# Optimization experiments

Measured on AMD Instinct MI355X. Metric: run time of the kernel, lower is better.

## Reference

```python
import jax, jax.numpy as jnp
import numpy as np

B, C, H, W = 32, 256, 32, 32


def setup_inputs() -> dict:
    key = jax.random.key(0)
    k1, k2, k3 = jax.random.split(key, 3)
    h = jax.random.normal(k1, (B, C, H, W), dtype=jnp.float32)
    w1_w = jax.random.normal(k2, (1, C), dtype=jnp.float32) * (1.0 / np.sqrt(C))
    w1_b = jnp.zeros((1,), dtype=jnp.float32)
    w2_w = jax.random.normal(k3, (1, C), dtype=jnp.float32) * (1.0 / np.sqrt(C))
    w2_b = jnp.zeros((1,), dtype=jnp.float32)
    return {"h": h, "w1_w": w1_w, "w1_b": w1_b, "w2_w": w2_w, "w2_b": w2_b}


def reference(h, w1_w, w1_b, w2_w, w2_b):
    b, c, hh, ww = h.shape
    x = jnp.transpose(h, (0, 2, 3, 1))            # [B,H,W,C]
    # scalar projections of every spatial token
    a = jnp.einsum('bhwc,c->bhw', x, w1_w[0]) + w1_b[0]   # query-side scalar [B,H,W]
    k = jnp.einsum('bhwc,c->bhw', x, w2_w[0]) + w2_b[0]   # key-side scalar   [B,H,W]
    n = hh * ww
    # additive attention scores over all spatial pairs: [B,H,W,HW]
    scores = jnp.tanh(a[:, :, :, None] + k.reshape(b, 1, 1, n))
    attn = jax.nn.softmax(scores, axis=-1)                 # exp(tanh)/sum == softmax(tanh)
    ctx = jnp.einsum('bijn,bnc->bijc', attn, x.reshape(b, n, c))  # [B,H,W,C]
    out = jnp.where(ctx >= 0, ctx, 0.2 * ctx)              # LeakyReLU(0.2)
    return jnp.transpose(out, (0, 3, 1, 2))                # [B,C,H,W]
```

## Files before the change

### kernel.cpp

```cpp
#include <hip/hip_runtime.h>

constexpr int Bn = 32;
constexpr int Cn = 256;
constexpr int Nn = 1024;

constexpr float C2 = 2.8853900817779268f;
constexpr float K1 = 1.4426950408889634f;

typedef __bf16 v8bf  __attribute__((ext_vector_type(8)));
typedef float  v16f  __attribute__((ext_vector_type(16)));


__global__ __launch_bounds__(512) void prep_kernel(
    const float* __restrict__ h,
    const float* __restrict__ w1, const float* __restrict__ w1b,
    const float* __restrict__ w2, const float* __restrict__ w2b,
    float* __restrict__ pa_g, float* __restrict__ q_g,
    unsigned char* __restrict__ hbf)
{
    int blk = blockIdx.x;
    int xcd = blk & 7, idx = blk >> 3;
    int b   = xcd * 4 + (idx >> 4);
    int n0  = (idx & 15) * 64;
    int t = threadIdx.x, w = t >> 6, l = t & 63;
    int co = l >> 3, oct = l & 7;

    __shared__ float p1[8][64], p2[8][64];

    float s1[8], s2[8];
#pragma unroll
    for (int j = 0; j < 8; ++j) { s1[j] = 0.f; s2[j] = 0.f; }

    const float* hb = h + (size_t)b * Cn * Nn + n0 + oct * 8;
    int nt32 = (n0 >> 5) + (oct >> 2);
    unsigned char* nt_base = hbf + (size_t)(b * 32 + nt32) * 16384;
    int g = oct & 3;

#pragma unroll
    for (int it = 0; it < 4; ++it) {
        int c = it * 64 + w * 8 + co;
        const float* src = hb + (size_t)c * Nn;
        float4 va = *(const float4*)src;
        float4 vb = *(const float4*)(src + 4);
        float w1c = w1[c], w2c = w2[c];
        float v[8] = {va.x, va.y, va.z, va.w, vb.x, vb.y, vb.z, vb.w};
        union { __bf16 bx[8]; uint4 u4; } pk;
#pragma unroll
        for (int j = 0; j < 8; ++j) {
            s1[j] = fmaf(v[j], w1c, s1[j]);
            s2[j] = fmaf(v[j], w2c, s2[j]);
            pk.bx[j] = (__bf16)v[j];
        }
        *(uint4*)(nt_base + c * 64 + ((g ^ (c & 3)) << 4)) = pk.u4;
    }

#pragma unroll
    for (int m = 8; m <= 32; m <<= 1) {
#pragma unroll
        for (int j = 0; j < 8; ++j) {
            s1[j] += __shfl_xor(s1[j], m);
            s2[j] += __shfl_xor(s2[j], m);
        }
    }
    if (co == 0) {
#pragma unroll
        for (int j = 0; j < 8; ++j) {
            p1[w][oct * 8 + j] = s1[j];
            p2[w][oct * 8 + j] = s2[j];
        }
    }
    __syncthreads();
    if (t < 64) {
        float a = w1b[0], k = w2b[0];
#pragma unroll
        for (int ww = 0; ww < 8; ++ww) { a += p1[ww][t]; k += p2[ww][t]; }
        pa_g[b * Nn + n0 + t] = exp2f(C2 * a);
        q_g [b * Nn + n0 + t] = exp2f(C2 * k);
    }
}

constexpr int EST_OFF  = 0;
constexpr int QS_OFF   = 16384;
constexpr int SP_OFF   = 65792;
constexpr int SINV_OFF = 67840;
constexpr int CTX_SMEM = 68096;

__global__ __launch_bounds__(512, 4) void ctx_kernel(
    const unsigned char* __restrict__ hbf,
    const float* __restrict__ pa_g, const float* __restrict__ q_g,
    float* __restrict__ out)
{
    __shared__ alignas(16) unsigned char smem[CTX_SMEM];
    float* qs           = (float*)(smem + QS_OFF);
    float (*Sp)[64]     = (float(*)[64])(smem + SP_OFF);
    float* Sinv         = (float*)(smem + SINV_OFF);
    float (*comb)[257]  = (float(*)[257])smem;

    int blk = blockIdx.x;
    int xcd = blk & 7, slot = blk >> 3;
    int b   = xcd * 4 + (slot >> 4);
    int i0  = (slot & 15) * 64;

    int t = threadIdx.x, w = t >> 6, l = t & 63;
    int lm = l & 31, lh = l >> 5;
    int cq = w & 3, wq = w >> 2;

    const unsigned char* hbf_b = hbf + (size_t)b * 524288;

    for (int i = t; i < Nn; i += 512) qs[i] = q_g[b * Nn + i];
    float pav = pa_g[b * Nn + i0 + l];

    v16f acc[2][2];
#pragma unroll
    for (int x = 0; x < 2; ++x)
#pragma unroll
        for (int y = 0; y < 2; ++y)
#pragma unroll
            for (int r = 0; r < 16; ++r) acc[x][y][r] = 0.f;
    float Spart = 0.f;

    int est_sw = l * 128 + ((w ^ (l & 7)) << 4);

    int cB   = cq * 64 + lm;
    int m4   = cB & 3;
    int off0 = cB * 64 + ((lh ^ m4) << 4);
    int off1 = cB * 64 + (((2 + lh) ^ m4) << 4);

    __syncthreads();
    for (int tt = 0; tt < 16; ++tt) {
        unsigned char* est_base = smem + EST_OFF + ((tt & 1) << 13);
        const unsigned char* pt = hbf_b + (size_t)((wq << 4) + tt) * 16384;
        v8bf b00 = *(const v8bf*)(pt + off0);
        v8bf b01 = *(const v8bf*)(pt + off0 + 2048);
        v8bf b10 = *(const v8bf*)(pt + off1);
        v8bf b11 = *(const v8bf*)(pt + off1 + 2048);
        {
            int qb = wq * 512 + tt * 32 + cq * 8;
            float4 q0 = *(const float4*)&qs[qb];
            float4 q1 = *(const float4*)&qs[qb + 4];
            float qv[8] = {q0.x, q0.y, q0.z, q0.w, q1.x, q1.y, q1.z, q1.w};
            v8bf ev;
#pragma unroll
            for (int j = 0; j < 8; ++j) {
                float z = pav * qv[j];
                float r = __builtin_amdgcn_rcpf(1.f + z);
                float e = exp2f(fmaf(r, -2.f * K1, K1));
                __bf16 eb = (__bf16)e;
                ev[j] = eb;
                Spart += (float)eb;
            }
            *(v8bf*)(est_base + est_sw) = ev;
        }
        __syncthreads();
#pragma unroll
        for (int ks = 0; ks < 2; ++ks) {
            int gA = ((wq << 2) + (ks << 1) + lh) ^ (lm & 7);
            v8bf a0 = *(const v8bf*)(est_base + lm * 128        + (gA << 4));
            v8bf a1 = *(const v8bf*)(est_base + (32 + lm) * 128 + (gA << 4));
            v8bf b0 = ks ? b10 : b00;
            v8bf b1 = ks ? b11 : b01;
            acc[0][0] = __builtin_amdgcn_mfma_f32_32x32x16_bf16(a0, b0, acc[0][0], 0, 0, 0);
            acc[0][1] = __builtin_amdgcn_mfma_f32_32x32x16_bf16(a0, b1, acc[0][1], 0, 0, 0);
            acc[1][0] = __builtin_amdgcn_mfma_f32_32x32x16_bf16(a1, b0, acc[1][0], 0, 0, 0);
            acc[1][1] = __builtin_amdgcn_mfma_f32_32x32x16_bf16(a1, b1, acc[1][1], 0, 0, 0);
        }
    }

    Sp[w][l] = Spart;
    __syncthreads();
    if (t < 64) {
        float S = 0.f;
#pragma unroll
        for (int ww = 0; ww < 8; ++ww) S += Sp[ww][t];
        Sinv[t] = 1.f / S;
    }
    if (wq == 1) {
#pragma unroll
        for (int x = 0; x < 2; ++x)
#pragma unroll
            for (int y = 0; y < 2; ++y)
#pragma unroll
                for (int r = 0; r < 16; ++r) {
                    int rl = (r & 3) + 8 * (r >> 2) + 4 * lh;
                    comb[x * 32 + rl][cq * 64 + y * 32 + lm] = acc[x][y][r];
                }
    }
    __syncthreads();
    if (wq == 0) {
#pragma unroll
        for (int x = 0; x < 2; ++x)
#pragma unroll
            for (int y = 0; y < 2; ++y)
#pragma unroll
                for (int r = 0; r < 16; ++r) {
                    int rl  = (r & 3) + 8 * (r >> 2) + 4 * lh;
                    int row = x * 32 + rl;
                    int col = cq * 64 + y * 32 + lm;
                    float v = (acc[x][y][r] + comb[row][col]) * Sinv[row];
                    v = (v >= 0.f) ? v : 0.2f * v;
                    comb[row][col] = v;
                }
    }
    __syncthreads();
    float* ob = out + (size_t)b * Cn * Nn + i0;
#pragma unroll
    for (int p = 0; p < 8; ++p) {
        int slot = t + (p << 9);
        int c    = slot >> 4;
        int i4   = (slot & 15) << 2;
        float4 o;
        o.x = comb[i4 + 0][c];
        o.y = comb[i4 + 1][c];
        o.z = comb[i4 + 2][c];
        o.w = comb[i4 + 3][c];
        *(float4*)(ob + (size_t)c * Nn + i4) = o;
    }
}

extern "C" void kernel_launch(void* const* d_in, const int* in_sizes, int n_in,
                              void* d_out, int out_size, void* d_ws, size_t ws_size,
                              hipStream_t stream) {
    const float* h   = (const float*)d_in[0];
    const float* w1w = (const float*)d_in[1];
    const float* w1b = (const float*)d_in[2];
    const float* w2w = (const float*)d_in[3];
    const float* w2b = (const float*)d_in[4];
    float* out = (float*)d_out;

    float* pa_ws = (float*)d_ws;
    float* q_ws  = pa_ws + Bn * Nn;
    unsigned char* hbf = (unsigned char*)d_ws + 262144;

    prep_kernel<<<512, 512, 0, stream>>>(h, w1w, w1b, w2w, w2b, pa_ws, q_ws, hbf);
    ctx_kernel <<<512, 512, 0, stream>>>(hbf, pa_ws, q_ws, out);
}
```

Before: 120.1 us.

## Fuse prep and ctx kernels with per-batch atomic flag barrier

Merges the projection/bf16-conversion kernel and the attention-context kernel into one launch. Each batch has an atomic counter that its 16 blocks increment after writing their prep outputs, and each block spins (with sleep and a guard limit) until all 16 arrive. This removes one kernel launch and the gap between kernels. In exchange it adds a memset launch, spin-wait latency, and a dependence on all 16 blocks of a batch being co-resident, which the launch bounds are meant to provide.

```diff
diff --git a/kernel.cpp b/kernel.cpp
--- a/kernel.cpp
+++ b/kernel.cpp
@@ -11,97 +11,109 @@
 typedef float  v16f  __attribute__((ext_vector_type(16)));
 
 
-__global__ __launch_bounds__(512) void prep_kernel(
+constexpr int EST_OFF  = 0;
+constexpr int QS_OFF   = 16384;
+constexpr int SP_OFF   = 65792;
+constexpr int SINV_OFF = 67840;
+constexpr int CTX_SMEM = 68096;
+constexpr int P1_OFF   = 0;
+constexpr int P2_OFF   = 2048;
+
+__global__ __launch_bounds__(512, 4) void fused_kernel(
     const float* __restrict__ h,
     const float* __restrict__ w1, const float* __restrict__ w1b,
     const float* __restrict__ w2, const float* __restrict__ w2b,
     float* __restrict__ pa_g, float* __restrict__ q_g,
-    unsigned char* __restrict__ hbf)
+    unsigned char* __restrict__ hbf,
+    float* __restrict__ out,
+    unsigned int* __restrict__ flags)
 {
+    __shared__ alignas(16) unsigned char smem[CTX_SMEM];
+
     int blk = blockIdx.x;
     int xcd = blk & 7, idx = blk >> 3;
     int b   = xcd * 4 + (idx >> 4);
     int n0  = (idx & 15) * 64;
     int t = threadIdx.x, w = t >> 6, l = t & 63;
-    int co = l >> 3, oct = l & 7;
-
-    __shared__ float p1[8][64], p2[8][64];
-
-    float s1[8], s2[8];
-#pragma unroll
-    for (int j = 0; j < 8; ++j) { s1[j] = 0.f; s2[j] = 0.f; }
-
-    const float* hb = h + (size_t)b * Cn * Nn + n0 + oct * 8;
-    int nt32 = (n0 >> 5) + (oct >> 2);
-    unsigned char* nt_base = hbf + (size_t)(b * 32 + nt32) * 16384;
-    int g = oct & 3;
-
-#pragma unroll
-    for (int it = 0; it < 4; ++it) {
-        int c = it * 64 + w * 8 + co;
-        const float* src = hb + (size_t)c * Nn;
-        float4 va = *(const float4*)src;
-        float4 vb = *(const float4*)(src + 4);
-        float w1c = w1[c], w2c = w2[c];
-        float v[8] = {va.x, va.y, va.z, va.w, vb.x, vb.y, vb.z, vb.w};
-        union { __bf16 bx[8]; uint4 u4; } pk;
-#pragma unroll
-        for (int j = 0; j < 8; ++j) {
-            s1[j] = fmaf(v[j], w1c, s1[j]);
-            s2[j] = fmaf(v[j], w2c, s2[j]);
-            pk.bx[j] = (__bf16)v[j];
-        }
-        *(uint4*)(nt_base + c * 64 + ((g ^ (c & 3)) << 4)) = pk.u4;
-    }
-
-#pragma unroll
-    for (int m = 8; m <= 32; m <<= 1) {
-#pragma unroll
-        for (int j = 0; j < 8; ++j) {
-            s1[j] += __shfl_xor(s1[j], m);
-            s2[j] += __shfl_xor(s2[j], m);
-        }
-    }
-    if (co == 0) {
-#pragma unroll
-        for (int j = 0; j < 8; ++j) {
-            p1[w][oct * 8 + j] = s1[j];
-            p2[w][oct * 8 + j] = s2[j];
-        }
-    }
-    __syncthreads();
-    if (t < 64) {
-        float a = w1b[0], k = w2b[0];
-#pragma unroll
-        for (int ww = 0; ww < 8; ++ww) { a += p1[ww][t]; k += p2[ww][t]; }
-        pa_g[b * Nn + n0 + t] = exp2f(C2 * a);
-        q_g [b * Nn + n0 + t] = exp2f(C2 * k);
-    }
-}
-
-constexpr int EST_OFF  = 0;
-constexpr int QS_OFF   = 16384;
-constexpr int SP_OFF   = 65792;
-constexpr int SINV_OFF = 67840;
-constexpr int CTX_SMEM = 68096;
-
-__global__ __launch_bounds__(512, 4) void ctx_kernel(
-    const unsigned char* __restrict__ hbf,
-    const float* __restrict__ pa_g, const float* __restrict__ q_g,
-    float* __restrict__ out)
-{
-    __shared__ alignas(16) unsigned char smem[CTX_SMEM];
+
+    {
+        float (*p1)[64] = (float(*)[64])(smem + P1_OFF);
+        float (*p2)[64] = (float(*)[64])(smem + P2_OFF);
+        int co = l >> 3, oct = l & 7;
+
+        float s1[8], s2[8];
+#pragma unroll
+        for (int j = 0; j < 8; ++j) { s1[j] = 0.f; s2[j] = 0.f; }
+
+        const float* hb = h + (size_t)b * Cn * Nn + n0 + oct * 8;
+        int nt32 = (n0 >> 5) + (oct >> 2);
+        unsigned char* nt_base = hbf + (size_t)(b * 32 + nt32) * 16384;
+        int g = oct & 3;
+
+#pragma unroll
+        for (int it = 0; it < 4; ++it) {
+            int c = it * 64 + w * 8 + co;
+            const float* src = hb + (size_t)c * Nn;
+            float4 va = *(const float4*)src;
+            float4 vb = *(const float4*)(src + 4);
+            float w1c = w1[c], w2c = w2[c];
+            float v[8] = {va.x, va.y, va.z, va.w, vb.x, vb.y, vb.z, vb.w};
+            union { __bf16 bx[8]; uint4 u4; } pk;
+#pragma unroll
+            for (int j = 0; j < 8; ++j) {
+                s1[j] = fmaf(v[j], w1c, s1[j]);
+                s2[j] = fmaf(v[j], w2c, s2[j]);
+                pk.bx[j] = (__bf16)v[j];
+            }
+            *(uint4*)(nt_base + c * 64 + ((g ^ (c & 3)) << 4)) = pk.u4;
+        }
+
+#pragma unroll
+        for (int m = 8; m <= 32; m <<= 1) {
+#pragma unroll
+            for (int j = 0; j < 8; ++j) {
+                s1[j] += __shfl_xor(s1[j], m);
+                s2[j] += __shfl_xor(s2[j], m);
+            }
+        }
+        if (co == 0) {
+#pragma unroll
+            for (int j = 0; j < 8; ++j) {
+                p1[w][oct * 8 + j] = s1[j];
+                p2[w][oct * 8 + j] = s2[j];
+            }
+        }
+        __syncthreads();
+        if (t < 64) {
+            float a = w1b[0], k = w2b[0];
+#pragma unroll
+            for (int ww = 0; ww < 8; ++ww) { a += p1[ww][t]; k += p2[ww][t]; }
+            pa_g[b * Nn + n0 + t] = exp2f(C2 * a);
+            q_g [b * Nn + n0 + t] = exp2f(C2 * k);
+        }
+    }
+
+    if (t == 0) {
+        __hip_atomic_fetch_add(flags + b, 1u, __ATOMIC_RELEASE,
+                               __HIP_MEMORY_SCOPE_AGENT);
+        int guard = 0;
+        while (__hip_atomic_load(flags + b, __ATOMIC_RELAXED,
+                                 __HIP_MEMORY_SCOPE_AGENT) < 16u &&
+               guard < (1 << 22)) {
+            __builtin_amdgcn_s_sleep(8);
+            ++guard;
+        }
+        (void)__hip_atomic_load(flags + b, __ATOMIC_ACQUIRE,
+                                __HIP_MEMORY_SCOPE_AGENT);
+    }
+    __syncthreads();
+
     float* qs           = (float*)(smem + QS_OFF);
     float (*Sp)[64]     = (float(*)[64])(smem + SP_OFF);
     float* Sinv         = (float*)(smem + SINV_OFF);
     float (*comb)[257]  = (float(*)[257])smem;
 
-    int blk = blockIdx.x;
-    int xcd = blk & 7, slot = blk >> 3;
-    int b   = xcd * 4 + (slot >> 4);
-    int i0  = (slot & 15) * 64;
-
-    int t = threadIdx.x, w = t >> 6, l = t & 63;
+    int i0 = n0;
     int lm = l & 31, lh = l >> 5;
     int cq = w & 3, wq = w >> 2;
 
@@ -230,7 +242,9 @@
     float* pa_ws = (float*)d_ws;
     float* q_ws  = pa_ws + Bn * Nn;
     unsigned char* hbf = (unsigned char*)d_ws + 262144;
-
-    prep_kernel<<<512, 512, 0, stream>>>(h, w1w, w1b, w2w, w2b, pa_ws, q_ws, hbf);
-    ctx_kernel <<<512, 512, 0, stream>>>(hbf, pa_ws, q_ws, out);
+    unsigned int* flags = (unsigned int*)((unsigned char*)d_ws + 17039360);
+
+    hipMemsetAsync(flags, 0, Bn * sizeof(unsigned int), stream);
+    fused_kernel<<<512, 512, 0, stream>>>(h, w1w, w1b, w2w, w2b,
+                                          pa_ws, q_ws, hbf, out, flags);
 }
```

Result: slower. 157.2 us (+30.9%).
